# Optimization experiments

Hardware: AMD Instinct MI355X
Metric: run time of the kernel (lower is better)

## Reference

```python
import jax, jax.numpy as jnp
import numpy as np

N = 100000   # nodes
E = 1600000  # edges
IN = 128     # in_dim == hidden_dim
OUT = 64
MD = 16      # motif_dim
GH = 64      # gate hidden
TAU = 1.0
EPS = 1e-5


def setup_inputs() -> dict:
    key = jax.random.key(0)
    ks = jax.random.split(key, 8)
    return {
        "x": jax.random.normal(ks[0], (N, IN), jnp.float32),
        "motif_x": jax.random.normal(ks[1], (N, MD), jnp.float32),
        "edge_index": jax.random.randint(ks[2], (2, E), 0, N, jnp.int64),
        "gate_w1": jax.random.normal(ks[3], (4 * MD, GH), jnp.float32) * 0.05,
        "gate_b1": jnp.zeros((GH,), jnp.float32),
        "gate_w2": jax.random.normal(ks[4], (GH, 1), jnp.float32) * 0.05,
        "gate_b2": jnp.zeros((1,), jnp.float32),
        "conv_w": jax.random.normal(ks[5], (2, IN, IN), jnp.float32) * 0.05,
        "conv_b": jnp.zeros((2, IN), jnp.float32),
        "ln_g": jnp.ones((2, IN), jnp.float32),
        "ln_b": jnp.zeros((2, IN), jnp.float32),
        "head_w": jax.random.normal(ks[6], (IN, OUT), jnp.float32) * 0.05,
        "head_b": jnp.zeros((OUT,), jnp.float32),
    }


def reference(x, motif_x, edge_index, gate_w1, gate_b1, gate_w2, gate_b2,
              conv_w, conv_b, ln_g, ln_b, head_w, head_b):
    src, dst = edge_index[0], edge_index[1]

    # ---- EdgeGate: gather motif feats, small MLP, sigmoid gate per edge ----
    mu = motif_x[src]                      # [E, MD]
    mv = motif_x[dst]                      # [E, MD]
    feats = jnp.concatenate([mu, mv, jnp.abs(mu - mv), mu * mv], axis=1)  # [E, 4*MD]
    h = jax.nn.relu(feats @ gate_w1 + gate_b1)
    g = (h @ gate_w2 + gate_b2)[:, 0]
    gate = jnp.clip(jax.nn.sigmoid(g / TAU), 0.0, 1.0)  # [E]

    # ---- gcn_norm with self-loops (fill weight 1.0), shared across layers ----
    loops = jnp.arange(N, dtype=src.dtype)
    src_f = jnp.concatenate([src, loops])  # [E+N]
    dst_f = jnp.concatenate([dst, loops])
    w = jnp.concatenate([gate, jnp.ones((N,), gate.dtype)])
    deg = jax.ops.segment_sum(w, dst_f, num_segments=N)
    dinv = jnp.where(deg > 0, jax.lax.rsqrt(jnp.maximum(deg, EPS * 0 + 1e-30)), 0.0)
    dinv = jnp.where(deg > 0, deg ** -0.5, 0.0)
    norm = dinv[src_f] * w * dinv[dst_f]   # [E+N]

    # ---- 2 GCN layers: lin -> scatter-add -> bias -> LN -> relu -> residual ----
    for i in range(2):
        xw = x @ conv_w[i]                                   # [N, IN]
        msg = norm[:, None] * xw[src_f]                      # [E+N, IN]
        hh = jax.ops.segment_sum(msg, dst_f, num_segments=N) + conv_b[i]
        mean = jnp.mean(hh, axis=-1, keepdims=True)
        var = jnp.mean((hh - mean) ** 2, axis=-1, keepdims=True)
        hh = (hh - mean) * jax.lax.rsqrt(var + EPS) * ln_g[i] + ln_b[i]
        hh = jax.nn.relu(hh)
        x = x + hh                                           # residual (dims match)

    return x @ head_w + head_b             # [N, OUT]
```

## Files before the change

kernel.cpp:

```cpp
#include <hip/hip_runtime.h>
#include <cstdint>
#include <cstddef>

#define NN 100000
#define NE 1600000
#define IND 128
#define OUTD 64
#define MDIM 16
#define GHID 64
#define NPART 12500

typedef __attribute__((ext_vector_type(8))) short bf8_t;
typedef __attribute__((ext_vector_type(4))) float f4_t;
typedef unsigned short ushort_t;

__device__ inline unsigned f2bf_pack(float a, float b) {
    unsigned ua = __float_as_uint(a);
    unsigned ub = __float_as_uint(b);
    unsigned ra = (ua + 0x7fffu + ((ua >> 16) & 1u)) >> 16;
    unsigned rb = (ub + 0x7fffu + ((ub >> 16) & 1u)) >> 16;
    return ra | (rb << 16);
}
__device__ inline ushort_t f2bf1(float f) {
    unsigned u = __float_as_uint(f);
    return (ushort_t)((u + 0x7fffu + ((u >> 16) & 1u)) >> 16);
}
__device__ inline float2 bf2x(unsigned u) {
    return make_float2(__uint_as_float(u << 16),
                       __uint_as_float(u & 0xffff0000u));
}

__global__ __launch_bounds__(64) void k_detect(const void* ei, int* flag) {
    const unsigned long long* p = (const unsigned long long*)ei;
    int i = threadIdx.x;
    unsigned long long v = p[(size_t)i * (NE / 64)];
    bool hi0 = (v >> 32) == 0ull;
    unsigned long long b = __ballot(hi0);
    if (i == 0) *flag = (b == ~0ull) ? 1 : 0;
}

__global__ __launch_bounds__(256) void k_init(int* count) {
    int n = blockIdx.x * 256 + threadIdx.x;
    if (n < NN) count[n] = 0;
}

__global__ __launch_bounds__(256) void k_hist(const void* __restrict__ ei,
                                              const int* __restrict__ flag,
                                              int* __restrict__ count) {
    int e = blockIdx.x * 256 + threadIdx.x;
    if (e >= NE) return;
    int d = (*flag) ? (int)((const long long*)ei)[NE + e]
                    : ((const int*)ei)[NE + e];
    atomicAdd(&count[d], 1);
}

__global__ __launch_bounds__(256) void k_prep(const float* __restrict__ cw,
                                              const float* __restrict__ hw,
                                              const float* __restrict__ w1,
                                              unsigned* __restrict__ btf) {
    int i = blockIdx.x * 256 + threadIdx.x;
    if (i >= 22528) return;
    const float* W;
    int ncols, local, kk, nt;
    int w, lane;
    if (i < 16384) {
        W = cw + (i >> 13) * 16384; ncols = 128; local = i & 8191;
        w = local & 3; lane = (local >> 2) & 63;
        kk = (local >> 8) & 3; nt = local >> 10;
    } else if (i < 20480) {
        W = hw; ncols = 64; local = i - 16384;
        w = local & 3; lane = (local >> 2) & 63;
        kk = (local >> 8) & 3; nt = local >> 10;
    } else {
        W = w1; ncols = 64; local = i - 20480;
        w = local & 3; lane = (local >> 2) & 63;
        kk = (local >> 8) & 1; nt = local >> 9;
    }
    int n = nt * 16 + (lane & 15);
    int k = kk * 32 + (lane >> 4) * 8 + 2 * w;
    btf[i] = f2bf_pack(W[k * ncols + n], W[(k + 1) * ncols + n]);
}

__global__ __launch_bounds__(256) void k_scan1(const int* __restrict__ count,
                                               int* __restrict__ rs,
                                               int* __restrict__ bsum) {
    __shared__ int sd[256];
    int tid = threadIdx.x;
    int base = blockIdx.x * 2048 + tid * 8;
    int loc[8]; int s = 0;
#pragma unroll
    for (int i = 0; i < 8; i++) {
        int idx = base + i;
        int v = (idx < NN) ? count[idx] : 0;
        loc[i] = s; s += v;
    }
    sd[tid] = s; __syncthreads();
    for (int off = 1; off < 256; off <<= 1) {
        int t = (tid >= off) ? sd[tid - off] : 0;
        __syncthreads();
        sd[tid] += t;
        __syncthreads();
    }
    int texcl = sd[tid] - s;
    if (tid == 255) bsum[blockIdx.x] = sd[255];
#pragma unroll
    for (int i = 0; i < 8; i++) {
        int idx = base + i;
        if (idx < NN) rs[idx] = texcl + loc[i];
    }
}

__global__ __launch_bounds__(64) void k_scan2(const int* __restrict__ bsum,
                                              int* __restrict__ boffs) {
    int tid = threadIdx.x;
    int v = (tid < 49) ? bsum[tid] : 0;
    int x = v;
#pragma unroll
    for (int off = 1; off < 64; off <<= 1) {
        int t = __shfl_up(x, off, 64);
        if (tid >= off) x += t;
    }
    boffs[tid] = x - v;
}

__global__ __launch_bounds__(256) void k_scan3(int* __restrict__ rs,
                                               const int* __restrict__ boffs,
                                               int* __restrict__ cursor) {
    int i = blockIdx.x * 256 + threadIdx.x;
    if (i < NN) {
        int v = rs[i] + boffs[i >> 11];
        rs[i] = v;
        cursor[i] = v;
    }
}

__global__ __launch_bounds__(256) void k_fill(const void* __restrict__ ei,
                                              const int* __restrict__ flag,
                                              int* __restrict__ cursor,
                                              int2* __restrict__ es) {
    int p = blockIdx.x & 7;
    int base = (blockIdx.x >> 3) * 2048;
    bool is64 = (*flag) != 0;
#pragma unroll 1
    for (int it = 0; it < 8; it++) {
        int e = base + it * 256 + threadIdx.x;
        if (e >= NE) break;
        int d = is64 ? (int)((const long long*)ei)[NE + e]
                     : ((const int*)ei)[NE + e];
        if ((unsigned)d / NPART != (unsigned)p) continue;
        int s = is64 ? (int)((const long long*)ei)[e] : ((const int*)ei)[e];
        int pos = atomicAdd(&cursor[d], 1);
        es[pos] = make_int2(s, d);
    }
}

__global__ __launch_bounds__(256) void k_gate(
    const float* __restrict__ motif, const int2* __restrict__ es,
    const uint4* __restrict__ w1f, const float* __restrict__ b1,
    const float* __restrict__ w2, const float* __restrict__ b2,
    float* __restrict__ g_s) {
    int wv = threadIdx.x >> 6, lane = threadIdx.x & 63;
    int e0 = (blockIdx.x * 4 + wv) * 16;
    int quad = lane >> 4, lx = lane & 15;
    int2 sd = es[e0 + lx];
    int node = (quad < 2) ? sd.x : sd.y;
    int half = quad & 1;
    const float4* mp =
        (const float4*)(motif + (size_t)node * MDIM + half * 8);
    float4 v0 = mp[0], v1 = mp[1];
    float own[8] = {v0.x, v0.y, v0.z, v0.w, v1.x, v1.y, v1.z, v1.w};
    union { unsigned u[4]; bf8_t v; } a0, a1;
#pragma unroll
    for (int q = 0; q < 4; q++) a0.u[q] = f2bf_pack(own[2 * q], own[2 * q + 1]);
    float f[8];
#pragma unroll
    for (int j = 0; j < 8; j++) {
        float oth = __shfl_xor(own[j], 32, 64);
        f[j] = (quad < 2) ? fabsf(own[j] - oth) : own[j] * oth;
    }
#pragma unroll
    for (int q = 0; q < 4; q++) a1.u[q] = f2bf_pack(f[2 * q], f[2 * q + 1]);
    f4_t acc[4];
#pragma unroll
    for (int nt = 0; nt < 4; nt++) {
        float bi = b1[nt * 16 + lx];
        acc[nt] = (f4_t){bi, bi, bi, bi};
    }
#pragma unroll
    for (int nt = 0; nt < 4; nt++) {
        union { uint4 u; bf8_t v; } b0, bb1;
        b0.u = w1f[(nt * 2 + 0) * 64 + lane];
        bb1.u = w1f[(nt * 2 + 1) * 64 + lane];
        acc[nt] = __builtin_amdgcn_mfma_f32_16x16x32_bf16(a0.v, b0.v, acc[nt],
                                                          0, 0, 0);
        acc[nt] = __builtin_amdgcn_mfma_f32_16x16x32_bf16(a1.v, bb1.v, acc[nt],
                                                          0, 0, 0);
    }
    float p[4] = {0.f, 0.f, 0.f, 0.f};
#pragma unroll
    for (int nt = 0; nt < 4; nt++) {
        float w2v = w2[nt * 16 + lx];
#pragma unroll
        for (int r = 0; r < 4; r++)
            p[r] = fmaf(fmaxf(acc[nt][r], 0.0f), w2v, p[r]);
    }
#pragma unroll
    for (int m = 1; m < 16; m <<= 1) {
#pragma unroll
        for (int r = 0; r < 4; r++) p[r] += __shfl_xor(p[r], m, 64);
    }
    if (lx < 4) {
        float g = p[lx] + b2[0];
        g_s[e0 + quad * 4 + lx] = 1.0f / (1.0f + __expf(-g));
    }
}

__global__ __launch_bounds__(256) void k_deg(const int* __restrict__ rowstart,
                                             const int* __restrict__ count,
                                             const float* __restrict__ g_s,
                                             float* __restrict__ dinv) {
    int n = blockIdx.x * 4 + (threadIdx.x >> 6);
    int lane = threadIdx.x & 63;
    if (n >= NN) return;
    int a = rowstart[n], cnt = count[n];
    float sum = 0.0f;
    for (int c = lane; c < cnt; c += 64) sum += g_s[a + c];
#pragma unroll
    for (int m = 1; m < 64; m <<= 1) sum += __shfl_xor(sum, m, 64);
    if (lane == 0) dinv[n] = rsqrtf(1.0f + sum);
}

__global__ __launch_bounds__(256) void k_wnorm(const int2* __restrict__ es,
                                               const float* __restrict__ dinv,
                                               float* __restrict__ g_s) {
    int e = blockIdx.x * 256 + threadIdx.x;
    if (e >= NE) return;
    int2 sd = es[e];
    g_s[e] *= dinv[sd.x] * dinv[sd.y];
}

__global__ __launch_bounds__(256) void k_mm_conv_f32(
    const float* __restrict__ A, const uint4* __restrict__ btf,
    ushort_t* __restrict__ outb) {
    int w = threadIdx.x >> 6, lane = threadIdx.x & 63;
    int mh = w & 1, nh = w >> 1;
    int quad = lane >> 4, lx = lane & 15;
    int m0 = blockIdx.x * 64 + mh * 32;
    bf8_t a[2][4];
#pragma unroll
    for (int mt = 0; mt < 2; mt++) {
        int row = m0 + mt * 16 + lx;
        row = row < NN ? row : NN - 1;
#pragma unroll
        for (int kk = 0; kk < 4; kk++) {
            const float4* ap =
                (const float4*)(A + (size_t)row * 128 + kk * 32 + quad * 8);
            float4 u0 = ap[0], u1 = ap[1];
            union { unsigned u[4]; bf8_t v; } t;
            t.u[0] = f2bf_pack(u0.x, u0.y);
            t.u[1] = f2bf_pack(u0.z, u0.w);
            t.u[2] = f2bf_pack(u1.x, u1.y);
            t.u[3] = f2bf_pack(u1.z, u1.w);
            a[mt][kk] = t.v;
        }
    }
    f4_t acc[2][4];
#pragma unroll
    for (int mt = 0; mt < 2; mt++)
#pragma unroll
        for (int nt = 0; nt < 4; nt++) acc[mt][nt] = (f4_t){0.f, 0.f, 0.f, 0.f};
#pragma unroll
    for (int nt = 0; nt < 4; nt++) {
        int ntg = nh * 4 + nt;
#pragma unroll
        for (int kk = 0; kk < 4; kk++) {
            union { uint4 u; bf8_t v; } bb;
            bb.u = btf[(ntg * 4 + kk) * 64 + lane];
            acc[0][nt] = __builtin_amdgcn_mfma_f32_16x16x32_bf16(
                a[0][kk], bb.v, acc[0][nt], 0, 0, 0);
            acc[1][nt] = __builtin_amdgcn_mfma_f32_16x16x32_bf16(
                a[1][kk], bb.v, acc[1][nt], 0, 0, 0);
        }
    }
#pragma unroll
    for (int mt = 0; mt < 2; mt++)
#pragma unroll
        for (int nt = 0; nt < 4; nt++) {
#pragma unroll
            for (int r = 0; r < 4; r++) {
                int row = m0 + mt * 16 + quad * 4 + r;
                if (row < NN)
                    outb[(size_t)row * 128 + (nh * 4 + nt) * 16 + lx] =
                        f2bf1(acc[mt][nt][r]);
            }
        }
}

__global__ __launch_bounds__(256) void k_mm_conv(
    const ushort_t* __restrict__ A, const uint4* __restrict__ btf,
    ushort_t* __restrict__ outb) {
    int w = threadIdx.x >> 6, lane = threadIdx.x & 63;
    int mh = w & 1, nh = w >> 1;
    int quad = lane >> 4, lx = lane & 15;
    int m0 = blockIdx.x * 64 + mh * 32;
    bf8_t a[2][4];
#pragma unroll
    for (int mt = 0; mt < 2; mt++) {
        int row = m0 + mt * 16 + lx;
        row = row < NN ? row : NN - 1;
#pragma unroll
        for (int kk = 0; kk < 4; kk++)
            a[mt][kk] = *(const bf8_t*)(A + (size_t)row * 128 + kk * 32 + quad * 8);
    }
    f4_t acc[2][4];
#pragma unroll
    for (int mt = 0; mt < 2; mt++)
#pragma unroll
        for (int nt = 0; nt < 4; nt++) acc[mt][nt] = (f4_t){0.f, 0.f, 0.f, 0.f};
#pragma unroll
    for (int nt = 0; nt < 4; nt++) {
        int ntg = nh * 4 + nt;
#pragma unroll
        for (int kk = 0; kk < 4; kk++) {
            union { uint4 u; bf8_t v; } bb;
            bb.u = btf[(ntg * 4 + kk) * 64 + lane];
            acc[0][nt] = __builtin_amdgcn_mfma_f32_16x16x32_bf16(
                a[0][kk], bb.v, acc[0][nt], 0, 0, 0);
            acc[1][nt] = __builtin_amdgcn_mfma_f32_16x16x32_bf16(
                a[1][kk], bb.v, acc[1][nt], 0, 0, 0);
        }
    }
#pragma unroll
    for (int mt = 0; mt < 2; mt++)
#pragma unroll
        for (int nt = 0; nt < 4; nt++) {
#pragma unroll
            for (int r = 0; r < 4; r++) {
                int row = m0 + mt * 16 + quad * 4 + r;
                if (row < NN)
                    outb[(size_t)row * 128 + (nh * 4 + nt) * 16 + lx] =
                        f2bf1(acc[mt][nt][r]);
            }
        }
}

__global__ __launch_bounds__(256) void k_mm_head(
    const ushort_t* __restrict__ A, const uint4* __restrict__ btf,
    const float* __restrict__ bias, float* __restrict__ out) {
    int w = threadIdx.x >> 6, lane = threadIdx.x & 63;
    int mh = w & 1, nh = w >> 1;
    int quad = lane >> 4, lx = lane & 15;
    int m0 = blockIdx.x * 64 + mh * 32;
    bf8_t a[2][4];
#pragma unroll
    for (int mt = 0; mt < 2; mt++) {
        int row = m0 + mt * 16 + lx;
        row = row < NN ? row : NN - 1;
#pragma unroll
        for (int kk = 0; kk < 4; kk++)
            a[mt][kk] = *(const bf8_t*)(A + (size_t)row * 128 + kk * 32 + quad * 8);
    }
    f4_t acc[2][2];
#pragma unroll
    for (int mt = 0; mt < 2; mt++)
#pragma unroll
        for (int nt = 0; nt < 2; nt++) acc[mt][nt] = (f4_t){0.f, 0.f, 0.f, 0.f};
#pragma unroll
    for (int nt = 0; nt < 2; nt++) {
        int ntg = nh * 2 + nt;
#pragma unroll
        for (int kk = 0; kk < 4; kk++) {
            union { uint4 u; bf8_t v; } bb;
            bb.u = btf[(ntg * 4 + kk) * 64 + lane];
            acc[0][nt] = __builtin_amdgcn_mfma_f32_16x16x32_bf16(
                a[0][kk], bb.v, acc[0][nt], 0, 0, 0);
            acc[1][nt] = __builtin_amdgcn_mfma_f32_16x16x32_bf16(
                a[1][kk], bb.v, acc[1][nt], 0, 0, 0);
        }
    }
#pragma unroll
    for (int mt = 0; mt < 2; mt++)
#pragma unroll
        for (int nt = 0; nt < 2; nt++) {
            int col = (nh * 2 + nt) * 16 + lx;
            float bs = bias[col];
#pragma unroll
            for (int r = 0; r < 4; r++) {
                int row = m0 + mt * 16 + quad * 4 + r;
                if (row < NN) out[(size_t)row * 64 + col] = acc[mt][nt][r] + bs;
            }
        }
}

__global__ __launch_bounds__(256) void k_aggr(
    const int* __restrict__ rowstart, const int* __restrict__ count,
    const int2* __restrict__ es, const float* __restrict__ w_s,
    const unsigned* __restrict__ xwb, const float* __restrict__ dinv,
    const float* __restrict__ xold, float* __restrict__ xnew,
    unsigned* __restrict__ xnewb, const float* __restrict__ cb,
    const float* __restrict__ lg, const float* __restrict__ lb) {
    int n = blockIdx.x * 4 + (threadIdx.x >> 6);
    int lane = threadIdx.x & 63;
    if (n >= NN) return;
    float dn = dinv[n];
    float2 acc = bf2x(xwb[(size_t)n * 64 + lane]);
    acc.x *= dn * dn; acc.y *= dn * dn;
    int start = rowstart[n], cnt = count[n];
    for (int c = 0; c < cnt; c += 64) {
        int rem = cnt - c;
        int sv = 0; float wv = 0.0f;
        if (lane < rem) {
            sv = es[start + c + lane].x;
            wv = w_s[start + c + lane];
        }
        int m = rem < 64 ? rem : 64;
        int j = 0;
        for (; j + 4 <= m; j += 4) {
            int s0 = __shfl(sv, j, 64), s1 = __shfl(sv, j + 1, 64);
            int s2 = __shfl(sv, j + 2, 64), s3 = __shfl(sv, j + 3, 64);
            float w0 = __shfl(wv, j, 64), w1 = __shfl(wv, j + 1, 64);
            float w2 = __shfl(wv, j + 2, 64), w3 = __shfl(wv, j + 3, 64);
            unsigned u0 = xwb[(size_t)s0 * 64 + lane];
            unsigned u1 = xwb[(size_t)s1 * 64 + lane];
            unsigned u2 = xwb[(size_t)s2 * 64 + lane];
            unsigned u3 = xwb[(size_t)s3 * 64 + lane];
            float2 v0 = bf2x(u0), v1 = bf2x(u1), v2 = bf2x(u2), v3 = bf2x(u3);
            acc.x = fmaf(w0, v0.x, acc.x); acc.y = fmaf(w0, v0.y, acc.y);
            acc.x = fmaf(w1, v1.x, acc.x); acc.y = fmaf(w1, v1.y, acc.y);
            acc.x = fmaf(w2, v2.x, acc.x); acc.y = fmaf(w2, v2.y, acc.y);
            acc.x = fmaf(w3, v3.x, acc.x); acc.y = fmaf(w3, v3.y, acc.y);
        }
        for (; j < m; j++) {
            int s = __shfl(sv, j, 64);
            float w = __shfl(wv, j, 64);
            float2 v = bf2x(xwb[(size_t)s * 64 + lane]);
            acc.x = fmaf(w, v.x, acc.x); acc.y = fmaf(w, v.y, acc.y);
        }
    }
    float2 cbv = ((const float2*)cb)[lane];
    acc.x += cbv.x; acc.y += cbv.y;
    float s1 = acc.x + acc.y, s2 = acc.x * acc.x + acc.y * acc.y;
#pragma unroll
    for (int mm = 1; mm < 64; mm <<= 1) {
        s1 += __shfl_xor(s1, mm, 64);
        s2 += __shfl_xor(s2, mm, 64);
    }
    float mean = s1 * (1.0f / 128.0f);
    float var = s2 * (1.0f / 128.0f) - mean * mean;
    float rstd = rsqrtf(var + 1e-5f);
    float2 lgv = ((const float2*)lg)[lane];
    float2 lbv = ((const float2*)lb)[lane];
    float y0 = fmaxf((acc.x - mean) * rstd * lgv.x + lbv.x, 0.0f);
    float y1 = fmaxf((acc.y - mean) * rstd * lgv.y + lbv.y, 0.0f);
    float2 xo = ((const float2*)xold)[(size_t)n * 64 + lane];
    float o0 = xo.x + y0, o1 = xo.y + y1;
    ((float2*)xnew)[(size_t)n * 64 + lane] = make_float2(o0, o1);
    xnewb[(size_t)n * 64 + lane] = f2bf_pack(o0, o1);
}

extern "C" void kernel_launch(void* const* d_in, const int* in_sizes, int n_in,
                              void* d_out, int out_size, void* d_ws,
                              size_t ws_size, hipStream_t stream) {
    const float* x = (const float*)d_in[0];
    const float* motif = (const float*)d_in[1];
    const void* ei = d_in[2];
    const float* gw1 = (const float*)d_in[3];
    const float* gb1 = (const float*)d_in[4];
    const float* gw2 = (const float*)d_in[5];
    const float* gb2 = (const float*)d_in[6];
    const float* cw = (const float*)d_in[7];
    const float* cb = (const float*)d_in[8];
    const float* lg = (const float*)d_in[9];
    const float* lb = (const float*)d_in[10];
    const float* hw = (const float*)d_in[11];
    const float* hb = (const float*)d_in[12];
    float* out = (float*)d_out;

    float* ws = (float*)d_ws;
    size_t o = 0;
    float* dinv = ws + o; o += NN;
    int* flag = (int*)(ws + o); o += 64;
    int* count = (int*)(ws + o); o += NN;
    int* rowstart = (int*)(ws + o); o += NN;
    int* cursor = (int*)(ws + o); o += NN;
    int* bsum = (int*)(ws + o); o += 64;
    int* boffs = (int*)(ws + o); o += 64;
    int2* es = (int2*)(ws + o); o += 2 * (size_t)NE;
    float* g_s = ws + o; o += NE;
    unsigned* xwb = (unsigned*)(ws + o); o += (size_t)NN * 64;
    float* xc = ws + o; o += (size_t)NN * IND;
    unsigned* xcb = (unsigned*)(ws + o); o += (size_t)NN * 64;
    unsigned* btf = (unsigned*)(ws + o); o += 22528;

    k_detect<<<1, 64, 0, stream>>>(ei, flag);
    k_init<<<(NN + 255) / 256, 256, 0, stream>>>(count);
    k_hist<<<NE / 256, 256, 0, stream>>>(ei, flag, count);
    k_prep<<<88, 256, 0, stream>>>(cw, hw, gw1, btf);

    k_scan1<<<(NN + 2047) / 2048, 256, 0, stream>>>(count, rowstart, bsum);
    k_scan2<<<1, 64, 0, stream>>>(bsum, boffs);
    k_scan3<<<(NN + 255) / 256, 256, 0, stream>>>(rowstart, boffs, cursor);
    k_fill<<<8 * ((NE + 2047) / 2048), 256, 0, stream>>>(ei, flag, cursor, es);

    k_gate<<<NE / 64, 256, 0, stream>>>(motif, es, (const uint4*)(btf + 20480),
                                        gb1, gw2, gb2, g_s);
    k_deg<<<(NN + 3) / 4, 256, 0, stream>>>(rowstart, count, g_s, dinv);
    k_wnorm<<<NE / 256, 256, 0, stream>>>(es, dinv, g_s);

    const int gmm = (NN + 63) / 64;
    k_mm_conv_f32<<<gmm, 256, 0, stream>>>(x, (const uint4*)btf,
                                           (ushort_t*)xwb);
    k_aggr<<<(NN + 3) / 4, 256, 0, stream>>>(rowstart, count, es, g_s, xwb,
                                             dinv, x, xc, xcb, cb, lg, lb);
    k_mm_conv<<<gmm, 256, 0, stream>>>((const ushort_t*)xcb,
                                       (const uint4*)(btf + 8192),
                                       (ushort_t*)xwb);
    k_aggr<<<(NN + 3) / 4, 256, 0, stream>>>(rowstart, count, es, g_s, xwb,
                                             dinv, xc, xc, xcb, cb + IND,
                                             lg + IND, lb + IND);

    k_mm_head<<<gmm, 256, 0, stream>>>((const ushort_t*)xcb,
                                       (const uint4*)(btf + 16384), hb, out);
}
```

Before: 555.0 us.

## Restructure aggregation into 4 edge groups with 16-byte gathers; precompute int32 edges

The aggregation kernel now splits each wavefront into four 16-lane groups. Each group handles a different edge and gathers the full 256-byte bf16 row with uint4 loads, and a cross-group shuffle reduction follows. This replaces one edge per wave with 4-byte loads and is meant to raise memory-level parallelism and cut instruction count. Edge indices are also converted once to int32 arrays, which k_fill then reads instead of the 64-bit input. The second layer skips the unused f32 store. Nontemporal loads and stores are used for streamed data.

```diff
diff --git a/kernel.cpp b/kernel.cpp
--- a/kernel.cpp
+++ b/kernel.cpp
@@ -12,6 +12,7 @@
 
 typedef __attribute__((ext_vector_type(8))) short bf8_t;
 typedef __attribute__((ext_vector_type(4))) float f4_t;
+typedef __attribute__((ext_vector_type(4))) unsigned int u4_t;
 typedef unsigned short ushort_t;
 
 __device__ inline unsigned f2bf_pack(float a, float b) {
@@ -44,13 +45,23 @@
     if (n < NN) count[n] = 0;
 }
 
-__global__ __launch_bounds__(256) void k_hist(const void* __restrict__ ei,
-                                              const int* __restrict__ flag,
-                                              int* __restrict__ count) {
+__global__ __launch_bounds__(256) void k_cvt(const void* __restrict__ ei,
+                                             const int* __restrict__ flag,
+                                             int* __restrict__ s32,
+                                             int* __restrict__ d32,
+                                             int* __restrict__ count) {
     int e = blockIdx.x * 256 + threadIdx.x;
     if (e >= NE) return;
-    int d = (*flag) ? (int)((const long long*)ei)[NE + e]
-                    : ((const int*)ei)[NE + e];
+    int s, d;
+    if (*flag) {
+        s = (int)((const long long*)ei)[e];
+        d = (int)((const long long*)ei)[NE + e];
+    } else {
+        s = ((const int*)ei)[e];
+        d = ((const int*)ei)[NE + e];
+    }
+    s32[e] = s;
+    d32[e] = d;
     atomicAdd(&count[d], 1);
 }
 
@@ -134,21 +145,19 @@
     }
 }
 
-__global__ __launch_bounds__(256) void k_fill(const void* __restrict__ ei,
-                                              const int* __restrict__ flag,
+__global__ __launch_bounds__(256) void k_fill(const int* __restrict__ s32,
+                                              const int* __restrict__ d32,
                                               int* __restrict__ cursor,
                                               int2* __restrict__ es) {
     int p = blockIdx.x & 7;
     int base = (blockIdx.x >> 3) * 2048;
-    bool is64 = (*flag) != 0;
 #pragma unroll 1
     for (int it = 0; it < 8; it++) {
         int e = base + it * 256 + threadIdx.x;
         if (e >= NE) break;
-        int d = is64 ? (int)((const long long*)ei)[NE + e]
-                     : ((const int*)ei)[NE + e];
+        int d = d32[e];
         if ((unsigned)d / NPART != (unsigned)p) continue;
-        int s = is64 ? (int)((const long long*)ei)[e] : ((const int*)ei)[e];
+        int s = s32[e];
         int pos = atomicAdd(&cursor[d], 1);
         es[pos] = make_int2(s, d);
     }
@@ -395,67 +404,109 @@
 __global__ __launch_bounds__(256) void k_aggr(
     const int* __restrict__ rowstart, const int* __restrict__ count,
     const int2* __restrict__ es, const float* __restrict__ w_s,
-    const unsigned* __restrict__ xwb, const float* __restrict__ dinv,
+    const uint4* __restrict__ xwb4, const float* __restrict__ dinv,
     const float* __restrict__ xold, float* __restrict__ xnew,
-    unsigned* __restrict__ xnewb, const float* __restrict__ cb,
-    const float* __restrict__ lg, const float* __restrict__ lb) {
+    uint4* __restrict__ xnewb4, const float* __restrict__ cb,
+    const float* __restrict__ lg, const float* __restrict__ lb,
+    const int store_f32) {
     int n = blockIdx.x * 4 + (threadIdx.x >> 6);
     int lane = threadIdx.x & 63;
     if (n >= NN) return;
+    int g = lane >> 4, lx = lane & 15;
     float dn = dinv[n];
-    float2 acc = bf2x(xwb[(size_t)n * 64 + lane]);
-    acc.x *= dn * dn; acc.y *= dn * dn;
+    float acc[8];
+#pragma unroll
+    for (int j = 0; j < 8; j++) acc[j] = 0.0f;
+    if (g == 0) {
+        uint4 u = xwb4[(size_t)n * 16 + lx];
+        float w = dn * dn;
+        float2 p0 = bf2x(u.x), p1 = bf2x(u.y), p2 = bf2x(u.z), p3 = bf2x(u.w);
+        acc[0] = w * p0.x; acc[1] = w * p0.y;
+        acc[2] = w * p1.x; acc[3] = w * p1.y;
+        acc[4] = w * p2.x; acc[5] = w * p2.y;
+        acc[6] = w * p3.x; acc[7] = w * p3.y;
+    }
     int start = rowstart[n], cnt = count[n];
-    for (int c = 0; c < cnt; c += 64) {
-        int rem = cnt - c;
-        int sv = 0; float wv = 0.0f;
-        if (lane < rem) {
-            sv = es[start + c + lane].x;
-            wv = w_s[start + c + lane];
-        }
-        int m = rem < 64 ? rem : 64;
-        int j = 0;
-        for (; j + 4 <= m; j += 4) {
-            int s0 = __shfl(sv, j, 64), s1 = __shfl(sv, j + 1, 64);
-            int s2 = __shfl(sv, j + 2, 64), s3 = __shfl(sv, j + 3, 64);
-            float w0 = __shfl(wv, j, 64), w1 = __shfl(wv, j + 1, 64);
-            float w2 = __shfl(wv, j + 2, 64), w3 = __shfl(wv, j + 3, 64);
-            unsigned u0 = xwb[(size_t)s0 * 64 + lane];
-            unsigned u1 = xwb[(size_t)s1 * 64 + lane];
-            unsigned u2 = xwb[(size_t)s2 * 64 + lane];
-            unsigned u3 = xwb[(size_t)s3 * 64 + lane];
-            float2 v0 = bf2x(u0), v1 = bf2x(u1), v2 = bf2x(u2), v3 = bf2x(u3);
-            acc.x = fmaf(w0, v0.x, acc.x); acc.y = fmaf(w0, v0.y, acc.y);
-            acc.x = fmaf(w1, v1.x, acc.x); acc.y = fmaf(w1, v1.y, acc.y);
-            acc.x = fmaf(w2, v2.x, acc.x); acc.y = fmaf(w2, v2.y, acc.y);
-            acc.x = fmaf(w3, v3.x, acc.x); acc.y = fmaf(w3, v3.y, acc.y);
-        }
-        for (; j < m; j++) {
-            int s = __shfl(sv, j, 64);
-            float w = __shfl(wv, j, 64);
-            float2 v = bf2x(xwb[(size_t)s * 64 + lane]);
-            acc.x = fmaf(w, v.x, acc.x); acc.y = fmaf(w, v.y, acc.y);
-        }
-    }
-    float2 cbv = ((const float2*)cb)[lane];
-    acc.x += cbv.x; acc.y += cbv.y;
-    float s1 = acc.x + acc.y, s2 = acc.x * acc.x + acc.y * acc.y;
-#pragma unroll
-    for (int mm = 1; mm < 64; mm <<= 1) {
-        s1 += __shfl_xor(s1, mm, 64);
-        s2 += __shfl_xor(s2, mm, 64);
+    for (int c0 = 0; c0 < cnt; c0 += 16) {
+        int sv[4]; float wv[4];
+#pragma unroll
+        for (int u = 0; u < 4; u++) {
+            int c = c0 + 4 * u + g;
+            bool ok = (c < cnt);
+            int e = start + (ok ? c : 0);
+            unsigned long long sd = __builtin_nontemporal_load(
+                (const unsigned long long*)&es[e]);
+            sv[u] = ok ? (int)(unsigned)sd : n;
+            wv[u] = ok ? __builtin_nontemporal_load(&w_s[e]) : 0.0f;
+        }
+        uint4 uu[4];
+#pragma unroll
+        for (int u = 0; u < 4; u++) uu[u] = xwb4[(size_t)sv[u] * 16 + lx];
+#pragma unroll
+        for (int u = 0; u < 4; u++) {
+            float w = wv[u];
+            float2 p0 = bf2x(uu[u].x), p1 = bf2x(uu[u].y);
+            float2 p2 = bf2x(uu[u].z), p3 = bf2x(uu[u].w);
+            acc[0] = fmaf(w, p0.x, acc[0]); acc[1] = fmaf(w, p0.y, acc[1]);
+            acc[2] = fmaf(w, p1.x, acc[2]); acc[3] = fmaf(w, p1.y, acc[3]);
+            acc[4] = fmaf(w, p2.x, acc[4]); acc[5] = fmaf(w, p2.y, acc[5]);
+            acc[6] = fmaf(w, p3.x, acc[6]); acc[7] = fmaf(w, p3.y, acc[7]);
+        }
+    }
+#pragma unroll
+    for (int j = 0; j < 8; j++) {
+        acc[j] += __shfl_xor(acc[j], 16, 64);
+        acc[j] += __shfl_xor(acc[j], 32, 64);
+    }
+    const float4* cb4 = (const float4*)cb;
+    float4 cbv0 = cb4[lx * 2], cbv1 = cb4[lx * 2 + 1];
+    acc[0] += cbv0.x; acc[1] += cbv0.y; acc[2] += cbv0.z; acc[3] += cbv0.w;
+    acc[4] += cbv1.x; acc[5] += cbv1.y; acc[6] += cbv1.z; acc[7] += cbv1.w;
+    float s1 = 0.0f, s2 = 0.0f;
+#pragma unroll
+    for (int j = 0; j < 8; j++) { s1 += acc[j]; s2 += acc[j] * acc[j]; }
+#pragma unroll
+    for (int m = 1; m < 16; m <<= 1) {
+        s1 += __shfl_xor(s1, m, 64);
+        s2 += __shfl_xor(s2, m, 64);
     }
     float mean = s1 * (1.0f / 128.0f);
     float var = s2 * (1.0f / 128.0f) - mean * mean;
     float rstd = rsqrtf(var + 1e-5f);
-    float2 lgv = ((const float2*)lg)[lane];
-    float2 lbv = ((const float2*)lb)[lane];
-    float y0 = fmaxf((acc.x - mean) * rstd * lgv.x + lbv.x, 0.0f);
-    float y1 = fmaxf((acc.y - mean) * rstd * lgv.y + lbv.y, 0.0f);
-    float2 xo = ((const float2*)xold)[(size_t)n * 64 + lane];
-    float o0 = xo.x + y0, o1 = xo.y + y1;
-    ((float2*)xnew)[(size_t)n * 64 + lane] = make_float2(o0, o1);
-    xnewb[(size_t)n * 64 + lane] = f2bf_pack(o0, o1);
+    const float4* lg4 = (const float4*)lg;
+    const float4* lb4 = (const float4*)lb;
+    float4 lgv0 = lg4[lx * 2], lgv1 = lg4[lx * 2 + 1];
+    float4 lbv0 = lb4[lx * 2], lbv1 = lb4[lx * 2 + 1];
+    float glv[8] = {lgv0.x, lgv0.y, lgv0.z, lgv0.w,
+                    lgv1.x, lgv1.y, lgv1.z, lgv1.w};
+    float blv[8] = {lbv0.x, lbv0.y, lbv0.z, lbv0.w,
+                    lbv1.x, lbv1.y, lbv1.z, lbv1.w};
+    const f4_t* xo4 = (const f4_t*)(xold + (size_t)n * 128 + lx * 8);
+    f4_t xov0 = __builtin_nontemporal_load(xo4);
+    f4_t xov1 = __builtin_nontemporal_load(xo4 + 1);
+    float xov[8] = {xov0.x, xov0.y, xov0.z, xov0.w,
+                    xov1.x, xov1.y, xov1.z, xov1.w};
+    float o[8];
+#pragma unroll
+    for (int j = 0; j < 8; j++) {
+        float y = fmaxf((acc[j] - mean) * rstd * glv[j] + blv[j], 0.0f);
+        o[j] = xov[j] + y;
+    }
+    if (g == 0 && store_f32) {
+        f4_t* xn4 = (f4_t*)(xnew + (size_t)n * 128 + lx * 8);
+        f4_t st0 = {o[0], o[1], o[2], o[3]};
+        f4_t st1 = {o[4], o[5], o[6], o[7]};
+        __builtin_nontemporal_store(st0, xn4);
+        __builtin_nontemporal_store(st1, xn4 + 1);
+    }
+    if (g == 1) {
+        uint4 pb;
+        pb.x = f2bf_pack(o[0], o[1]);
+        pb.y = f2bf_pack(o[2], o[3]);
+        pb.z = f2bf_pack(o[4], o[5]);
+        pb.w = f2bf_pack(o[6], o[7]);
+        xnewb4[(size_t)n * 16 + lx] = pb;
+    }
 }
 
 extern "C" void kernel_launch(void* const* d_in, const int* in_sizes, int n_in,
@@ -492,15 +543,18 @@
     unsigned* xcb = (unsigned*)(ws + o); o += (size_t)NN * 64;
     unsigned* btf = (unsigned*)(ws + o); o += 22528;
 
+    int* s32 = (int*)xc;
+    int* d32 = (int*)xc + NE;
+
     k_detect<<<1, 64, 0, stream>>>(ei, flag);
     k_init<<<(NN + 255) / 256, 256, 0, stream>>>(count);
-    k_hist<<<NE / 256, 256, 0, stream>>>(ei, flag, count);
+    k_cvt<<<NE / 256, 256, 0, stream>>>(ei, flag, s32, d32, count);
     k_prep<<<88, 256, 0, stream>>>(cw, hw, gw1, btf);
 
     k_scan1<<<(NN + 2047) / 2048, 256, 0, stream>>>(count, rowstart, bsum);
     k_scan2<<<1, 64, 0, stream>>>(bsum, boffs);
     k_scan3<<<(NN + 255) / 256, 256, 0, stream>>>(rowstart, boffs, cursor);
-    k_fill<<<8 * ((NE + 2047) / 2048), 256, 0, stream>>>(ei, flag, cursor, es);
+    k_fill<<<8 * ((NE + 2047) / 2048), 256, 0, stream>>>(s32, d32, cursor, es);
 
     k_gate<<<NE / 64, 256, 0, stream>>>(motif, es, (const uint4*)(btf + 20480),
                                         gb1, gw2, gb2, g_s);
@@ -510,14 +564,16 @@
     const int gmm = (NN + 63) / 64;
     k_mm_conv_f32<<<gmm, 256, 0, stream>>>(x, (const uint4*)btf,
                                            (ushort_t*)xwb);
-    k_aggr<<<(NN + 3) / 4, 256, 0, stream>>>(rowstart, count, es, g_s, xwb,
-                                             dinv, x, xc, xcb, cb, lg, lb);
+    k_aggr<<<(NN + 3) / 4, 256, 0, stream>>>(rowstart, count, es, g_s,
+                                             (const uint4*)xwb, dinv, x, xc,
+                                             (uint4*)xcb, cb, lg, lb, 1);
     k_mm_conv<<<gmm, 256, 0, stream>>>((const ushort_t*)xcb,
                                        (const uint4*)(btf + 8192),
                                        (ushort_t*)xwb);
-    k_aggr<<<(NN + 3) / 4, 256, 0, stream>>>(rowstart, count, es, g_s, xwb,
-                                             dinv, xc, xc, xcb, cb + IND,
-                                             lg + IND, lb + IND);
+    k_aggr<<<(NN + 3) / 4, 256, 0, stream>>>(rowstart, count, es, g_s,
+                                             (const uint4*)xwb, dinv, xc, xc,
+                                             (uint4*)xcb, cb + IND, lg + IND,
+                                             lb + IND, 0);
 
     k_mm_head<<<gmm, 256, 0, stream>>>((const ushort_t*)xcb,
                                        (const uint4*)(btf + 16384), hb, out);
```

New measurement: 588.3 us. 6.0% more time.
